# Kernel optimization log

Hardware: AMD Instinct MI355X
Metric: run time of the kernel (lower is better)

The kernel has to match this reference:

```python
import jax, jax.numpy as jnp
import numpy as np

V, E, H, C = 50257, 256, 512, 16  # vocab, embed_dim, hidden_size, n_cells
B, T = 256, 128
LN_EPS = 1e-5


def setup_inputs() -> dict:
    key = jax.random.key(0)
    ks = jax.random.split(key, 16)
    s_h = 1.0 / np.sqrt(H)
    s_e = 1.0 / np.sqrt(E)
    return {
        "tokens": jax.random.randint(ks[0], (B, T), 0, V),
        "emb": jax.random.normal(ks[1], (V, E), jnp.float32) * 0.02,
        "Wproj": jax.random.normal(ks[2], (E, H), jnp.float32) * s_e,
        "bproj": jnp.zeros((H,), jnp.float32),
        "Wp": jax.random.normal(ks[3], (C, H, H), jnp.float32) * s_h,
        "bp": jnp.zeros((C, H), jnp.float32),
        "ln_g": jnp.ones((C, H), jnp.float32),
        "ln_b": jnp.zeros((C, H), jnp.float32),
        "Wih": jax.random.normal(ks[4], (C, 4 * H, H), jnp.float32) * s_h,
        "bih": jnp.zeros((C, 4 * H), jnp.float32),
        "Whh": jax.random.normal(ks[5], (C, 4 * H, H), jnp.float32) * s_h,
        "bhh": jnp.zeros((C, 4 * H), jnp.float32),
        "Wa": jax.random.normal(ks[6], (C, H, H), jnp.float32) * s_h,
        "ba": jnp.zeros((C, H), jnp.float32),
        "gate_logit": jnp.zeros((C,), jnp.float32),  # torch.tensor(0.0) per cell
    }


def _layernorm(x, g, b):
    mu = jnp.mean(x, axis=-1, keepdims=True)
    var = jnp.var(x, axis=-1, keepdims=True)
    return (x - mu) * jax.lax.rsqrt(var + LN_EPS) * g + b


def reference(tokens, emb, Wproj, bproj, Wp, bp, ln_g, ln_b,
              Wih, bih, Whh, bhh, Wa, ba, gate_logit):
    # embedding (padding_idx=0 zeroed) + projection to hidden size
    emb = emb.at[0].set(0.0)
    xs = emb[tokens] @ Wproj + bproj              # [B,T,H]
    xs = jnp.transpose(xs, (1, 0, 2))             # [T,B,H] for scan

    gate = jax.nn.sigmoid(gate_logit)[:, None, None]  # [C,1,1]

    def step(carry, x_t):
        h, c, ext = carry                          # h,c: [C,B,H], ext: [B,H]
        # input_adapter == Identity (input_size == hidden_size); external injection
        x = x_t[None] + 0.3 * ext[None]            # [C,B,H]
        # perception: Linear + ReLU + LayerNorm
        p = jax.nn.relu(jnp.einsum('cbh,chk->cbk', x, Wp) + bp[:, None, :])
        p = _layernorm(p, ln_g[:, None, :], ln_b[:, None, :])
        # LSTMCell (torch gate order i, f, g, o)
        gates = (jnp.einsum('cbh,cgh->cbg', p, Wih) + bih[:, None, :]
                 + jnp.einsum('cbh,cgh->cbg', h, Whh) + bhh[:, None, :])
        i_g, f_g, g_g, o_g = jnp.split(gates, 4, axis=-1)
        c_new = jax.nn.sigmoid(f_g) * c + jax.nn.sigmoid(i_g) * jnp.tanh(g_g)
        h_new = jax.nn.sigmoid(o_g) * jnp.tanh(c_new)
        # association + sigmoid gate
        a = jnp.tanh(jnp.einsum('cbh,chk->cbk', h_new, Wa) + ba[:, None, :])
        out = a * gate                             # [C,B,H]
        y = jnp.mean(out, axis=0)                  # aggregate cells -> [B,H]
        return (h_new, c_new, y), y

    h0 = jnp.zeros((C, B, H), xs.dtype)
    c0 = jnp.zeros((C, B, H), xs.dtype)
    ext0 = jnp.zeros((B, H), xs.dtype)
    _, ys = jax.lax.scan(step, (h0, c0, ext0), xs)  # ys: [T,B,H]
    return jnp.transpose(ys, (1, 0, 2))             # [B,T,H]
```

## Files before the change

### kernel.cpp

```cpp
#include <hip/hip_runtime.h>
#include <hip/hip_bf16.h>

#define V 50257
#define E 256
#define H 512
#define C 16
#define B 256
#define T 128

typedef _Float16 f16x8 __attribute__((ext_vector_type(8)));
typedef _Float16 f16x4 __attribute__((ext_vector_type(4)));
typedef float f32x4 __attribute__((ext_vector_type(4)));

__device__ __forceinline__ float sigm(float x) { return 1.0f / (1.0f + __expf(-x)); }

__device__ __forceinline__ void gload16(const _Float16* g, _Float16* l) {
  __builtin_amdgcn_global_load_lds((const __attribute__((address_space(1))) unsigned*)g,
                                   (__attribute__((address_space(3))) unsigned*)l, 16, 0, 0);
}

__global__ __launch_bounds__(256) void k_emb(const int* __restrict__ tokens,
                                             const float* __restrict__ emb,
                                             const float* __restrict__ Wproj,
                                             const float* __restrict__ bproj,
                                             _Float16* __restrict__ xs_h) {
  __shared__ float elds[16][256];
  const int tid = threadIdx.x;
  const int r0 = blockIdx.x * 16;
#pragma unroll
  for (int i = 0; i < 16; ++i) {
    int r = r0 + i;
    int t = r >> 8, b = r & 255;
    int tok = tokens[b * T + t];
    elds[i][tid] = (tok == 0) ? 0.0f : emb[(size_t)tok * E + tid];
  }
  __syncthreads();
  float acc0[16], acc1[16];
#pragma unroll
  for (int i = 0; i < 16; ++i) { acc0[i] = 0.0f; acc1[i] = 0.0f; }
  for (int k = 0; k < E; k += 4) {
    float w0[4], w1[4];
#pragma unroll
    for (int kk = 0; kk < 4; ++kk) {
      w0[kk] = Wproj[(k + kk) * H + tid];
      w1[kk] = Wproj[(k + kk) * H + tid + 256];
    }
#pragma unroll
    for (int i = 0; i < 16; ++i) {
      float4 e4 = *(const float4*)&elds[i][k];
      acc0[i] = fmaf(e4.x, w0[0], acc0[i]);
      acc0[i] = fmaf(e4.y, w0[1], acc0[i]);
      acc0[i] = fmaf(e4.z, w0[2], acc0[i]);
      acc0[i] = fmaf(e4.w, w0[3], acc0[i]);
      acc1[i] = fmaf(e4.x, w1[0], acc1[i]);
      acc1[i] = fmaf(e4.y, w1[1], acc1[i]);
      acc1[i] = fmaf(e4.z, w1[2], acc1[i]);
      acc1[i] = fmaf(e4.w, w1[3], acc1[i]);
    }
  }
  float bp0 = bproj[tid], bp1 = bproj[tid + 256];
#pragma unroll
  for (int i = 0; i < 16; ++i) {
    size_t r = (size_t)(r0 + i);
    xs_h[r * H + tid] = (_Float16)(acc0[i] + bp0);
    xs_h[r * H + tid + 256] = (_Float16)(acc1[i] + bp1);
  }
}

__global__ __launch_bounds__(256) void k_cvt_wg(const float* __restrict__ Wih,
                                                const float* __restrict__ Whh,
                                                _Float16* __restrict__ WgT) {
  for (size_t i4 = ((size_t)blockIdx.x * 256 + threadIdx.x) * 4; i4 < (size_t)33554432;
       i4 += (size_t)gridDim.x * 1024) {
    size_t c = i4 >> 21;
    size_t rem = i4 & 2097151;
    size_t np = rem >> 10;
    size_t k2 = rem & 1023;
    int gate = (int)((np >> 4) & 3);
    int hh = (int)(((np >> 6) << 4) | (np & 15));
    size_t n = (size_t)gate * 512 + hh;
    const float* src = (k2 < 512) ? (Wih + (c * 2048 + n) * 512 + k2)
                                  : (Whh + (c * 2048 + n) * 512 + (k2 - 512));
    float4 v = *(const float4*)src;
    f16x4 o;
    o[0] = (_Float16)v.x; o[1] = (_Float16)v.y; o[2] = (_Float16)v.z; o[3] = (_Float16)v.w;
    *(f16x4*)&WgT[i4] = o;
  }
}

__global__ __launch_bounds__(256) void k_cvt_tr(const float* __restrict__ W,
                                                _Float16* __restrict__ WT) {
  __shared__ float tl[64][65];
  const int tid = threadIdx.x;
  const int c = blockIdx.z;
  const int k0 = blockIdx.y * 64, n0 = blockIdx.x * 64;
  const float* Wc = W + (size_t)c * 262144;
#pragma unroll
  for (int q = 0; q < 16; ++q) {
    int idx = q * 256 + tid;
    int r = idx >> 6, cc = idx & 63;
    tl[r][cc] = Wc[(size_t)(k0 + r) * 512 + n0 + cc];
  }
  __syncthreads();
  _Float16* WTc = WT + (size_t)c * 262144;
#pragma unroll
  for (int q = 0; q < 16; ++q) {
    int idx = q * 256 + tid;
    int rr = idx >> 6, cc = idx & 63;
    WTc[(size_t)(n0 + rr) * 512 + k0 + cc] = (_Float16)tl[cc][rr];
  }
}

__global__ __launch_bounds__(256) void k_bias(const float* __restrict__ bih,
                                              const float* __restrict__ bhh,
                                              float* __restrict__ bsum) {
  int i = blockIdx.x * 256 + threadIdx.x;
  if (i < C * 4 * H) {
    int c = i >> 11, np = i & 2047;
    int gate = (np >> 4) & 3;
    int hh = ((np >> 6) << 4) | (np & 15);
    int n = gate * 512 + hh;
    bsum[i] = bih[c * 2048 + n] + bhh[c * 2048 + n];
  }
}

__global__ __launch_bounds__(256, 2) void k_pln(const _Float16* __restrict__ xq,
                                                const _Float16* __restrict__ WpT,
                                                const float* __restrict__ bp,
                                                const float* __restrict__ ln_g,
                                                const float* __restrict__ ln_b,
                                                _Float16* __restrict__ Pdst) {
  __shared__ _Float16 Bsl[512 * 64];
  const int tid = threadIdx.x;
  const int w = tid >> 6, l = tid & 63;
  const int mt = blockIdx.x;
  const int c = blockIdx.y;
  const int m0 = mt * 32;
  const _Float16* Bb = WpT + (size_t)c * 262144;
  const int srow = l >> 3, sj = l & 7;
  const int lm = l & 15, lk = l >> 4;
  f32x4 acc[2][8];
#pragma unroll
  for (int i = 0; i < 2; ++i)
#pragma unroll
    for (int j = 0; j < 8; ++j) acc[i][j] = (f32x4)0.0f;
  const _Float16* pA0 = xq + (size_t)(m0 + lm) * 512 + lk * 8;
  const _Float16* pA1 = pA0 + 16 * 512;
  f16x8 a0s0 = *(const f16x8*)pA0;
  f16x8 a0s1 = *(const f16x8*)(pA0 + 32);
  f16x8 a1s0 = *(const f16x8*)pA1;
  f16x8 a1s1 = *(const f16x8*)(pA1 + 32);
#pragma unroll 1
  for (int kb = 0; kb < 8; ++kb) {
#pragma unroll
    for (int q = 0; q < 16; ++q) {
      int r = q * 32 + w * 8 + srow;
      int gj = sj ^ (r & 7);
      gload16(Bb + (size_t)r * 512 + kb * 64 + gj * 8, &Bsl[(q * 32 + w * 8) * 64]);
    }
    f16x8 u00 = a0s0, u01 = a0s1, u10 = a1s0, u11 = a1s1;
    if (kb < 7) {
      a0s0 = *(const f16x8*)(pA0 + (kb + 1) * 64);
      a0s1 = *(const f16x8*)(pA0 + (kb + 1) * 64 + 32);
      a1s0 = *(const f16x8*)(pA1 + (kb + 1) * 64);
      a1s1 = *(const f16x8*)(pA1 + (kb + 1) * 64 + 32);
    }
    __syncthreads();
#pragma unroll
    for (int s2 = 0; s2 < 2; ++s2) {
      f16x8 bf[8];
#pragma unroll
      for (int j = 0; j < 8; ++j) {
        int RN = w * 128 + j * 16 + lm;
        int pn = (s2 * 4 + lk) ^ (RN & 7);
        bf[j] = *(const f16x8*)&Bsl[RN * 64 + pn * 8];
      }
      f16x8 ua = s2 ? u01 : u00;
      f16x8 ub = s2 ? u11 : u10;
#pragma unroll
      for (int j = 0; j < 8; ++j) {
        acc[0][j] = __builtin_amdgcn_mfma_f32_16x16x32_f16(ua, bf[j], acc[0][j], 0, 0, 0);
        acc[1][j] = __builtin_amdgcn_mfma_f32_16x16x32_f16(ub, bf[j], acc[1][j], 0, 0, 0);
      }
    }
    __syncthreads();
  }
  float bv[8], gcol[8], bcol[8];
#pragma unroll
  for (int j = 0; j < 8; ++j) {
    int col = w * 128 + j * 16 + lm;
    bv[j] = bp[c * 512 + col];
    gcol[j] = ln_g[c * 512 + col];
    bcol[j] = ln_b[c * 512 + col];
  }
  float vals[2][8][4];
  float s1l[2][4], s2l[2][4];
#pragma unroll
  for (int i = 0; i < 2; ++i)
#pragma unroll
    for (int rg = 0; rg < 4; ++rg) { s1l[i][rg] = 0.0f; s2l[i][rg] = 0.0f; }
#pragma unroll
  for (int i = 0; i < 2; ++i)
#pragma unroll
    for (int j = 0; j < 8; ++j)
#pragma unroll
      for (int rg = 0; rg < 4; ++rg) {
        float v = fmaxf(acc[i][j][rg] + bv[j], 0.0f);
        vals[i][j][rg] = v;
        s1l[i][rg] += v;
        s2l[i][rg] += v * v;
      }
#pragma unroll
  for (int m = 1; m < 16; m <<= 1) {
#pragma unroll
    for (int i = 0; i < 2; ++i)
#pragma unroll
      for (int rg = 0; rg < 4; ++rg) {
        s1l[i][rg] += __shfl_xor(s1l[i][rg], m, 64);
        s2l[i][rg] += __shfl_xor(s2l[i][rg], m, 64);
      }
  }
  float* st = (float*)Bsl;
  if (lm == 0) {
#pragma unroll
    for (int i = 0; i < 2; ++i)
#pragma unroll
      for (int rg = 0; rg < 4; ++rg) {
        int row = i * 16 + lk * 4 + rg;
        st[(w * 32 + row) * 2] = s1l[i][rg];
        st[(w * 32 + row) * 2 + 1] = s2l[i][rg];
      }
  }
  __syncthreads();
  float mu_[2][4], rs_[2][4];
#pragma unroll
  for (int i = 0; i < 2; ++i)
#pragma unroll
    for (int rg = 0; rg < 4; ++rg) {
      int row = i * 16 + lk * 4 + rg;
      float t1 = 0.0f, t2 = 0.0f;
#pragma unroll
      for (int ww = 0; ww < 4; ++ww) {
        t1 += st[(ww * 32 + row) * 2];
        t2 += st[(ww * 32 + row) * 2 + 1];
      }
      float mu = t1 * (1.0f / 512.0f);
      float var = t2 * (1.0f / 512.0f) - mu * mu;
      mu_[i][rg] = mu;
      rs_[i][rg] = rsqrtf(var + 1e-5f);
    }
#pragma unroll
  for (int i = 0; i < 2; ++i)
#pragma unroll
    for (int j = 0; j < 8; ++j) {
      int col = w * 128 + j * 16 + lm;
#pragma unroll
      for (int rg = 0; rg < 4; ++rg) {
        int row = i * 16 + lk * 4 + rg;
        float o = (vals[i][j][rg] - mu_[i][rg]) * rs_[i][rg] * gcol[j] + bcol[j];
        Pdst[((size_t)c * 256 + m0 + row) * 1024 + col] = (_Float16)o;
      }
    }
}

__global__ __launch_bounds__(256, 2) void k_gates(const _Float16* __restrict__ A,
                                                  const _Float16* __restrict__ Bm,
                                                  const float* __restrict__ bias,
                                                  float* __restrict__ cstate,
                                                  _Float16* __restrict__ hdst) {
  __shared__ _Float16 Asl[128 * 64];
  __shared__ _Float16 Bsl[128 * 64];
  const int tid = threadIdx.x;
  const int w = tid >> 6, l = tid & 63;
  const int c = blockIdx.z;
  const int m0 = blockIdx.y * 128, n0 = blockIdx.x * 128;
  const _Float16* Ab = A + (size_t)c * 262144 + (size_t)m0 * 1024;
  const _Float16* Bb = Bm + (size_t)c * 2097152 + (size_t)n0 * 1024;
  f32x4 acc[4][4];
#pragma unroll
  for (int i = 0; i < 4; ++i)
#pragma unroll
    for (int j = 0; j < 4; ++j) acc[i][j] = (f32x4)0.0f;
  const int wm = (w >> 1) * 64, wn = (w & 1) * 64;
  const int srow = l >> 3, sj = l & 7;
#pragma unroll 1
  for (int kb = 0; kb < 16; ++kb) {
#pragma unroll
    for (int q = 0; q < 4; ++q) {
      int r = w * 32 + q * 8 + srow;
      int gj = sj ^ (r & 7);
      gload16(Ab + (size_t)r * 1024 + kb * 64 + gj * 8, &Asl[(w * 32 + q * 8) * 64]);
      gload16(Bb + (size_t)r * 1024 + kb * 64 + gj * 8, &Bsl[(w * 32 + q * 8) * 64]);
    }
    __syncthreads();
#pragma unroll
    for (int s2 = 0; s2 < 2; ++s2) {
      f16x8 af[4], bf[4];
#pragma unroll
      for (int i = 0; i < 4; ++i) {
        int R = wm + i * 16 + (l & 15);
        int p = (s2 * 4 + (l >> 4)) ^ (R & 7);
        af[i] = *(const f16x8*)&Asl[R * 64 + p * 8];
        int RN = wn + i * 16 + (l & 15);
        int pn = (s2 * 4 + (l >> 4)) ^ (RN & 7);
        bf[i] = *(const f16x8*)&Bsl[RN * 64 + pn * 8];
      }
#pragma unroll
      for (int i = 0; i < 4; ++i)
#pragma unroll
        for (int j = 0; j < 4; ++j)
          acc[i][j] = __builtin_amdgcn_mfma_f32_16x16x32_f16(af[i], bf[j], acc[i][j], 0, 0, 0);
    }
    __syncthreads();
  }
  const int rl = (l >> 4) * 4, cl = l & 15;
  const int hh = (((n0 + wn) >> 6) << 4) + cl;
  float bv[4];
#pragma unroll
  for (int j = 0; j < 4; ++j) bv[j] = bias[(size_t)c * 2048 + (n0 + wn) + j * 16 + cl];
#pragma unroll
  for (int i = 0; i < 4; ++i) {
#pragma unroll
    for (int rg = 0; rg < 4; ++rg) {
      int row = m0 + wm + i * 16 + rl + rg;
      float ig = acc[i][0][rg] + bv[0];
      float fg = acc[i][1][rg] + bv[1];
      float gg = acc[i][2][rg] + bv[2];
      float og = acc[i][3][rg] + bv[3];
      size_t ci = ((size_t)c * 256 + row) * 512 + hh;
      float cn = sigm(fg) * cstate[ci] + sigm(ig) * tanhf(gg);
      cstate[ci] = cn;
      hdst[((size_t)c * 256 + row) * 1024 + 512 + hh] = (_Float16)(sigm(og) * tanhf(cn));
    }
  }
}

__global__ __launch_bounds__(256, 2) void k_assoc(const _Float16* __restrict__ An,
                                                  const _Float16* __restrict__ WaT,
                                                  const float* __restrict__ ba,
                                                  const float* __restrict__ gl,
                                                  _Float16* __restrict__ abuf) {
  __shared__ _Float16 Asl[64 * 64];
  __shared__ _Float16 Bsl[128 * 64];
  const int tid = threadIdx.x;
  const int w = tid >> 6, l = tid & 63;
  const int nt = blockIdx.x, mt = blockIdx.y, c = blockIdx.z;
  const int n0 = nt * 128;
  const _Float16* Ab = An + 512 + ((size_t)c * 256 + mt * 64) * 1024;
  const _Float16* Bb = WaT + (size_t)c * 262144 + (size_t)n0 * 512;
  f32x4 acc[2][4];
#pragma unroll
  for (int i = 0; i < 2; ++i)
#pragma unroll
    for (int j = 0; j < 4; ++j) acc[i][j] = (f32x4)0.0f;
  const int wm = (w >> 1) * 32, wn = (w & 1) * 64;
  const int srow = l >> 3, sj = l & 7;
  const int lm = l & 15, lk = l >> 4;
#pragma unroll 1
  for (int kb = 0; kb < 8; ++kb) {
#pragma unroll
    for (int q = 0; q < 2; ++q) {
      int r = q * 32 + w * 8 + srow;
      int gj = sj ^ (r & 7);
      gload16(Ab + (size_t)r * 1024 + kb * 64 + gj * 8, &Asl[(q * 32 + w * 8) * 64]);
    }
#pragma unroll
    for (int q = 0; q < 4; ++q) {
      int r = q * 32 + w * 8 + srow;
      int gj = sj ^ (r & 7);
      gload16(Bb + (size_t)r * 512 + kb * 64 + gj * 8, &Bsl[(q * 32 + w * 8) * 64]);
    }
    __syncthreads();
#pragma unroll
    for (int s2 = 0; s2 < 2; ++s2) {
      f16x8 af[2], bf[4];
#pragma unroll
      for (int i = 0; i < 2; ++i) {
        int R = wm + i * 16 + lm;
        int p = (s2 * 4 + lk) ^ (R & 7);
        af[i] = *(const f16x8*)&Asl[R * 64 + p * 8];
      }
#pragma unroll
      for (int j = 0; j < 4; ++j) {
        int RN = wn + j * 16 + lm;
        int pn = (s2 * 4 + lk) ^ (RN & 7);
        bf[j] = *(const f16x8*)&Bsl[RN * 64 + pn * 8];
      }
#pragma unroll
      for (int i = 0; i < 2; ++i)
#pragma unroll
        for (int j = 0; j < 4; ++j)
          acc[i][j] = __builtin_amdgcn_mfma_f32_16x16x32_f16(af[i], bf[j], acc[i][j], 0, 0, 0);
    }
    __syncthreads();
  }
  float gv = sigm(gl[c]);
#pragma unroll
  for (int i = 0; i < 2; ++i)
#pragma unroll
    for (int j = 0; j < 4; ++j) {
      int gc = n0 + wn + j * 16 + lm;
      float bav = ba[c * 512 + gc];
#pragma unroll
      for (int rg = 0; rg < 4; ++rg) {
        int row = mt * 64 + wm + i * 16 + lk * 4 + rg;
        float v = tanhf(acc[i][j][rg] + bav) * gv;
        abuf[(size_t)c * 131072 + (size_t)row * 512 + gc] = (_Float16)v;
      }
    }
}

__global__ __launch_bounds__(256) void k_agg(const _Float16* __restrict__ abuf,
                                             const _Float16* __restrict__ xs_h,
                                             _Float16* __restrict__ xq,
                                             float* __restrict__ out, int t) {
  int idx = blockIdx.x * 256 + threadIdx.x;
  int i4 = idx * 4;
  float s[4] = {0.0f, 0.0f, 0.0f, 0.0f};
#pragma unroll
  for (int c = 0; c < 16; ++c) {
    f16x4 a = *(const f16x4*)&abuf[(size_t)c * 131072 + i4];
#pragma unroll
    for (int j = 0; j < 4; ++j) s[j] += (float)a[j];
  }
  int b = i4 >> 9, h = i4 & 511;
  float4 y4;
  float* yp = &y4.x;
#pragma unroll
  for (int j = 0; j < 4; ++j) yp[j] = s[j] * (1.0f / 16.0f);
  *(float4*)&out[((size_t)b * T + t) * 512 + h] = y4;
  if (t + 1 < T) {
    f16x4 xs4 = *(const f16x4*)&xs_h[(size_t)(t + 1) * 131072 + i4];
    f16x4 xn;
#pragma unroll
    for (int j = 0; j < 4; ++j) xn[j] = (_Float16)((float)xs4[j] + 0.3f * yp[j]);
    *(f16x4*)&xq[i4] = xn;
  }
}

extern "C" void kernel_launch(void* const* d_in, const int* in_sizes, int n_in,
                              void* d_out, int out_size, void* d_ws, size_t ws_size,
                              hipStream_t stream) {
  const int* tokens = (const int*)d_in[0];
  const float* emb = (const float*)d_in[1];
  const float* Wproj = (const float*)d_in[2];
  const float* bproj = (const float*)d_in[3];
  const float* Wp = (const float*)d_in[4];
  const float* bp = (const float*)d_in[5];
  const float* ln_g = (const float*)d_in[6];
  const float* ln_b = (const float*)d_in[7];
  const float* Wih = (const float*)d_in[8];
  const float* bih = (const float*)d_in[9];
  const float* Whh = (const float*)d_in[10];
  const float* bhh = (const float*)d_in[11];
  const float* Wa = (const float*)d_in[12];
  const float* ba = (const float*)d_in[13];
  const float* gl = (const float*)d_in[14];
  float* out = (float*)d_out;

  char* w8 = (char*)d_ws;
  _Float16* xs_h = (_Float16*)w8;
  _Float16* Aq0 = (_Float16*)(w8 + 33554432);
  _Float16* Aq1 = (_Float16*)(w8 + 50331648);
  float* cbuf = (float*)(w8 + 67108864);
  _Float16* abuf = (_Float16*)(w8 + 75497472);
  _Float16* xq = (_Float16*)(w8 + 79691776);
  _Float16* WpT = (_Float16*)(w8 + 79953920);
  _Float16* WaT = (_Float16*)(w8 + 88342528);
  _Float16* WgT = (_Float16*)(w8 + 96731136);
  float* bsum = (float*)(w8 + 163840000);

  hipMemsetAsync(Aq0, 0, 16777216, stream);
  hipMemsetAsync(cbuf, 0, 8388608, stream);

  k_cvt_wg<<<4096, 256, 0, stream>>>(Wih, Whh, WgT);
  k_cvt_tr<<<dim3(8, 8, 16), 256, 0, stream>>>(Wp, WpT);
  k_cvt_tr<<<dim3(8, 8, 16), 256, 0, stream>>>(Wa, WaT);
  k_bias<<<128, 256, 0, stream>>>(bih, bhh, bsum);
  k_emb<<<T * B / 16, 256, 0, stream>>>(tokens, emb, Wproj, bproj, xs_h);
  hipMemcpyAsync(xq, xs_h, 262144, hipMemcpyDeviceToDevice, stream);

  for (int t = 0; t < T; ++t) {
    _Float16* Ac = (t & 1) ? Aq1 : Aq0;
    _Float16* An = (t & 1) ? Aq0 : Aq1;
    k_pln<<<dim3(8, 16), 256, 0, stream>>>(xq, WpT, bp, ln_g, ln_b, Ac);
    k_gates<<<dim3(16, 2, 16), 256, 0, stream>>>(Ac, WgT, bsum, cbuf, An);
    k_assoc<<<dim3(4, 4, 16), 256, 0, stream>>>(An, WaT, ba, gl, abuf);
    k_agg<<<128, 256, 0, stream>>>(abuf, xs_h, xq, out, t);
  }
}
```

Measured before the change: 8.433 ms.

## Retile gates GEMM to full-M 256x64 blocks and interleave cells across block index

```diff
diff --git a/kernel.cpp b/kernel.cpp
--- a/kernel.cpp
+++ b/kernel.cpp
@@ -133,8 +133,9 @@
   __shared__ _Float16 Bsl[512 * 64];
   const int tid = threadIdx.x;
   const int w = tid >> 6, l = tid & 63;
-  const int mt = blockIdx.x;
-  const int c = blockIdx.y;
+  const int blk = blockIdx.x;
+  const int c = blk & 15;
+  const int mt = blk >> 4;
   const int m0 = mt * 32;
   const _Float16* Bb = WpT + (size_t)c * 262144;
   const int srow = l >> 3, sj = l & 7;
@@ -268,29 +269,36 @@
                                                   const float* __restrict__ bias,
                                                   float* __restrict__ cstate,
                                                   _Float16* __restrict__ hdst) {
-  __shared__ _Float16 Asl[128 * 64];
-  __shared__ _Float16 Bsl[128 * 64];
+  __shared__ _Float16 Asl[256 * 64];
+  __shared__ _Float16 Bsl[64 * 64];
   const int tid = threadIdx.x;
   const int w = tid >> 6, l = tid & 63;
-  const int c = blockIdx.z;
-  const int m0 = blockIdx.y * 128, n0 = blockIdx.x * 128;
-  const _Float16* Ab = A + (size_t)c * 262144 + (size_t)m0 * 1024;
+  const int blk = blockIdx.x;
+  const int c = blk & 15;
+  const int n0 = (blk >> 4) * 64;
+  const _Float16* Ab = A + (size_t)c * 262144;
   const _Float16* Bb = Bm + (size_t)c * 2097152 + (size_t)n0 * 1024;
   f32x4 acc[4][4];
 #pragma unroll
   for (int i = 0; i < 4; ++i)
 #pragma unroll
     for (int j = 0; j < 4; ++j) acc[i][j] = (f32x4)0.0f;
-  const int wm = (w >> 1) * 64, wn = (w & 1) * 64;
+  const int wm = w * 64;
   const int srow = l >> 3, sj = l & 7;
+  const int lm = l & 15, lk = l >> 4;
 #pragma unroll 1
   for (int kb = 0; kb < 16; ++kb) {
 #pragma unroll
-    for (int q = 0; q < 4; ++q) {
-      int r = w * 32 + q * 8 + srow;
+    for (int q = 0; q < 8; ++q) {
+      int r = w * 64 + q * 8 + srow;
       int gj = sj ^ (r & 7);
-      gload16(Ab + (size_t)r * 1024 + kb * 64 + gj * 8, &Asl[(w * 32 + q * 8) * 64]);
-      gload16(Bb + (size_t)r * 1024 + kb * 64 + gj * 8, &Bsl[(w * 32 + q * 8) * 64]);
+      gload16(Ab + (size_t)r * 1024 + kb * 64 + gj * 8, &Asl[(w * 64 + q * 8) * 64]);
+    }
+#pragma unroll
+    for (int q = 0; q < 2; ++q) {
+      int r = w * 16 + q * 8 + srow;
+      int gj = sj ^ (r & 7);
+      gload16(Bb + (size_t)r * 1024 + kb * 64 + gj * 8, &Bsl[(w * 16 + q * 8) * 64]);
     }
     __syncthreads();
 #pragma unroll
@@ -298,12 +306,15 @@
       f16x8 af[4], bf[4];
 #pragma unroll
       for (int i = 0; i < 4; ++i) {
-        int R = wm + i * 16 + (l & 15);
-        int p = (s2 * 4 + (l >> 4)) ^ (R & 7);
+        int R = wm + i * 16 + lm;
+        int p = (s2 * 4 + lk) ^ (R & 7);
         af[i] = *(const f16x8*)&Asl[R * 64 + p * 8];
-        int RN = wn + i * 16 + (l & 15);
-        int pn = (s2 * 4 + (l >> 4)) ^ (RN & 7);
-        bf[i] = *(const f16x8*)&Bsl[RN * 64 + pn * 8];
+      }
+#pragma unroll
+      for (int j = 0; j < 4; ++j) {
+        int RN = j * 16 + lm;
+        int pn = (s2 * 4 + lk) ^ (RN & 7);
+        bf[j] = *(const f16x8*)&Bsl[RN * 64 + pn * 8];
       }
 #pragma unroll
       for (int i = 0; i < 4; ++i)
@@ -313,16 +324,16 @@
     }
     __syncthreads();
   }
-  const int rl = (l >> 4) * 4, cl = l & 15;
-  const int hh = (((n0 + wn) >> 6) << 4) + cl;
+  const int rl = lk * 4, cl = lm;
+  const int hh = ((n0 >> 6) << 4) + cl;
   float bv[4];
 #pragma unroll
-  for (int j = 0; j < 4; ++j) bv[j] = bias[(size_t)c * 2048 + (n0 + wn) + j * 16 + cl];
+  for (int j = 0; j < 4; ++j) bv[j] = bias[(size_t)c * 2048 + n0 + j * 16 + cl];
 #pragma unroll
   for (int i = 0; i < 4; ++i) {
 #pragma unroll
     for (int rg = 0; rg < 4; ++rg) {
-      int row = m0 + wm + i * 16 + rl + rg;
+      int row = wm + i * 16 + rl + rg;
       float ig = acc[i][0][rg] + bv[0];
       float fg = acc[i][1][rg] + bv[1];
       float gg = acc[i][2][rg] + bv[2];
@@ -344,7 +355,10 @@
   __shared__ _Float16 Bsl[128 * 64];
   const int tid = threadIdx.x;
   const int w = tid >> 6, l = tid & 63;
-  const int nt = blockIdx.x, mt = blockIdx.y, c = blockIdx.z;
+  const int blk = blockIdx.x;
+  const int c = blk & 15;
+  const int r_ = blk >> 4;
+  const int nt = r_ & 3, mt = r_ >> 2;
   const int n0 = nt * 128;
   const _Float16* Ab = An + 512 + ((size_t)c * 256 + mt * 64) * 1024;
   const _Float16* Bb = WaT + (size_t)c * 262144 + (size_t)n0 * 512;
@@ -483,9 +497,9 @@
   for (int t = 0; t < T; ++t) {
     _Float16* Ac = (t & 1) ? Aq1 : Aq0;
     _Float16* An = (t & 1) ? Aq0 : Aq1;
-    k_pln<<<dim3(8, 16), 256, 0, stream>>>(xq, WpT, bp, ln_g, ln_b, Ac);
-    k_gates<<<dim3(16, 2, 16), 256, 0, stream>>>(Ac, WgT, bsum, cbuf, An);
-    k_assoc<<<dim3(4, 4, 16), 256, 0, stream>>>(An, WaT, ba, gl, abuf);
+    k_pln<<<128, 256, 0, stream>>>(xq, WpT, bp, ln_g, ln_b, Ac);
+    k_gates<<<512, 256, 0, stream>>>(Ac, WgT, bsum, cbuf, An);
+    k_assoc<<<256, 256, 0, stream>>>(An, WaT, ba, gl, abuf);
     k_agg<<<128, 256, 0, stream>>>(abuf, xs_h, xq, out, t);
   }
 }
```

Result: faster. 7.816 ms (-7.3%).
